# Kernel tuning notes

Measured on AMD Instinct MI355X. Metric: run time of the kernel, lower is better.

Reference implementation:

```python
import jax, jax.numpy as jnp
import numpy as np

IN_CH, OUT_CH = 32, 32
MODES1, MODES2 = 16, 16
B, H, W = 16, 256, 256


def setup_inputs() -> dict:
    key = jax.random.key(0)
    k1, k2, k3 = jax.random.split(key, 3)
    scale = 1.0 / (IN_CH * OUT_CH)
    x = jax.random.normal(k1, (B, IN_CH, H, W), dtype=jnp.float32)
    # weights stored as real view of complex: [..., 2] = (real, imag)
    w1 = scale * jax.random.uniform(k2, (IN_CH, OUT_CH, MODES1, MODES2, 2), dtype=jnp.float32)
    w2 = scale * jax.random.uniform(k3, (IN_CH, OUT_CH, MODES1, MODES2, 2), dtype=jnp.float32)
    return {"x": x, "w1": w1, "w2": w2}


def reference(x, w1, w2):
    m1, m2 = MODES1, MODES2
    b, _, h, w = x.shape
    x_ft = jnp.fft.rfft2(x, axes=(-2, -1))  # [B, in_ch, H, W//2+1] complex
    c1 = w1[..., 0] + 1j * w1[..., 1]       # [in_ch, out_ch, m1, m2]
    c2 = w2[..., 0] + 1j * w2[..., 1]
    o1 = jnp.einsum('bixy,ioxy->boxy', x_ft[:, :, :m1, :m2], c1)
    o2 = jnp.einsum('bixy,ioxy->boxy', x_ft[:, :, -m1:, :m2], c2)
    out_ft = jnp.zeros((b, c1.shape[1], h, w // 2 + 1), dtype=x_ft.dtype)
    out_ft = out_ft.at[:, :, :m1, :m2].set(o1)
    out_ft = out_ft.at[:, :, -m1:, :m2].set(o2)
    return jnp.fft.irfft2(out_ft, s=(h, w), axes=(-2, -1))
```

## Files before the change

kernel.cpp:

```cpp
#include <hip/hip_runtime.h>
#include <math.h>

#define BB 16
#define CC 32
#define HH 256
#define WW 256
#define NIMG (BB * CC)

typedef _Float16 f16;
typedef __attribute__((ext_vector_type(8))) _Float16 f16x8;
typedef __attribute__((ext_vector_type(4))) float f32x4;

constexpr float TWO_PI_OVER_256 = 6.28318530717958647692f / 256.0f;

#define N_TWF 8192
#define N_ACOL 32768
#define N_AINV 16384
#define N_BINV 8192

static __device__ __forceinline__ f32x4 mfma3(f16x8 ah, f16x8 al, f16x8 bh,
                                              f16x8 bl, f32x4 c) {
  c = __builtin_amdgcn_mfma_f32_16x16x32_f16(ah, bh, c, 0, 0, 0);
  c = __builtin_amdgcn_mfma_f32_16x16x32_f16(ah, bl, c, 0, 0, 0);
  c = __builtin_amdgcn_mfma_f32_16x16x32_f16(al, bh, c, 0, 0, 0);
  return c;
}

static __device__ __forceinline__ void split16(float v, f16* hi, f16* lo) {
  f16 h_ = (f16)v;
  *hi = h_;
  *lo = (f16)(v - (float)h_);
}

__global__ __launch_bounds__(256) void k_tw(f16* __restrict__ fb) {
  const int id = blockIdx.x * 256 + threadIdx.x;
  f16* twf_hi = fb;
  f16* twf_lo = twf_hi + N_TWF;
  f16* acol_hi = twf_lo + N_TWF;
  f16* acol_lo = acol_hi + N_ACOL;
  f16* ainv_hi = acol_lo + N_ACOL;
  f16* ainv_lo = ainv_hi + N_AINV;
  f16* binv_hi = ainv_lo + N_AINV;
  f16* binv_lo = binv_hi + N_BINV;

  float v;
  f16 *dh, *dl;
  if (id < N_TWF) {
    int idx = id;
    int j = idx & 7, lane = (idx >> 3) & 63, ks = (idx >> 9) & 7,
        nt = (idx >> 12) & 1;
    int col = nt * 16 + (lane & 15);
    int w = ks * 32 + ((lane >> 4) << 3) + j;
    int kx = col >> 1, ri = col & 1;
    int ph = (kx * w) & 255;
    float s, c;
    sincosf(TWO_PI_OVER_256 * (float)ph, &s, &c);
    v = ri ? -s : c;
    dh = twf_hi + idx;
    dl = twf_lo + idx;
  } else if (id < N_TWF + N_ACOL) {
    int idx = id - N_TWF;
    int j = idx & 7, lane = (idx >> 3) & 63, ks = (idx >> 9) & 7,
        mt = (idx >> 12) & 3, half = (idx >> 14) & 1;
    int row = mt * 16 + (lane & 15);
    int k = ks * 32 + ((lane >> 4) << 3) + j;
    int h = half * 128 + (k >> 1);
    int rj = k & 1;
    int zr = (row < 32) ? row : row - 32;
    int ky = (zr < 16) ? zr : 224 + zr;
    int ph = (ky * h) & 255;
    float s, c;
    sincosf(TWO_PI_OVER_256 * (float)ph, &s, &c);
    if (row < 32)
      v = rj ? s : c;
    else
      v = rj ? c : -s;
    dh = acol_hi + idx;
    dl = acol_lo + idx;
  } else if (id < N_TWF + N_ACOL + N_AINV) {
    int idx = id - N_TWF - N_ACOL;
    int j = idx & 7, lane = (idx >> 3) & 63, ks = (idx >> 9) & 1,
        mt = (idx >> 10) & 15;
    int h = mt * 16 + (lane & 15);
    int k = ks * 32 + ((lane >> 4) << 3) + j;
    int zr = k >> 1, rj = k & 1;
    int ky = (zr < 16) ? zr : 224 + zr;
    int ph = (ky * h) & 255;
    float s, c;
    sincosf(TWO_PI_OVER_256 * (float)ph, &s, &c);
    v = rj ? s : c;
    dh = ainv_hi + idx;
    dl = ainv_lo + idx;
  } else {
    int idx = id - N_TWF - N_ACOL - N_AINV;
    int j = idx & 7, lane = (idx >> 3) & 63, nt = (idx >> 9) & 15;
    int w = nt * 16 + (lane & 15);
    int k = ((lane >> 4) << 3) + j;
    int kx = k >> 1, ri = k & 1;
    int ph = (kx * w) & 255;
    float s, c;
    sincosf(TWO_PI_OVER_256 * (float)ph, &s, &c);
    float scale = ((kx == 0) ? 1.0f : 2.0f) / 65536.0f;
    v = ri ? -scale * s : scale * c;
    dh = binv_hi + idx;
    dl = binv_lo + idx;
  }
  f16 hi, lo;
  split16(v, &hi, &lo);
  *dh = hi;
  *dl = lo;
}

__global__ __launch_bounds__(256) void k_fwd(const float* __restrict__ x,
                                             const f16* __restrict__ twf_hi,
                                             const f16* __restrict__ twf_lo,
                                             const f16* __restrict__ acol_hi,
                                             const f16* __restrict__ acol_lo,
                                             float* __restrict__ Zp) {
  __shared__ __align__(16) f16 Yc_hi[16 * 260];
  __shared__ __align__(16) f16 Yc_lo[16 * 260];
  const int t = threadIdx.x, lane = t & 63, wid = t >> 6;
  const int l15 = lane & 15, kgrp = lane >> 4;
  const int img = blockIdx.x >> 1;
  const int half = blockIdx.x & 1;
  const float* xim = x + (size_t)img * (HH * WW) + half * 128 * WW;

  for (int r = 0; r < 2; ++r) {
    const int mt = r * 4 + wid;
    f32x4 acc0 = {0.f, 0.f, 0.f, 0.f}, acc1 = {0.f, 0.f, 0.f, 0.f};
    const float* ap = xim + (mt * 16 + l15) * WW + kgrp * 8;
    float4 st[16];
#pragma unroll
    for (int ks = 0; ks < 8; ++ks) {
      st[2 * ks] = *(const float4*)(ap + ks * 32);
      st[2 * ks + 1] = *(const float4*)(ap + ks * 32 + 4);
    }
#pragma unroll
    for (int ks = 0; ks < 8; ++ks) {
      float vv[8] = {st[2 * ks].x,     st[2 * ks].y,     st[2 * ks].z,
                     st[2 * ks].w,     st[2 * ks + 1].x, st[2 * ks + 1].y,
                     st[2 * ks + 1].z, st[2 * ks + 1].w};
      f16x8 ah, al;
#pragma unroll
      for (int e = 0; e < 8; ++e) {
        f16 h_ = (f16)vv[e];
        ah[e] = h_;
        al[e] = (f16)(vv[e] - (float)h_);
      }
      const int b0 = ((0 * 8 + ks) * 64 + lane) * 8;
      const int b1 = ((1 * 8 + ks) * 64 + lane) * 8;
      f16x8 b0h = *(const f16x8*)(twf_hi + b0);
      f16x8 b0l = *(const f16x8*)(twf_lo + b0);
      f16x8 b1h = *(const f16x8*)(twf_hi + b1);
      f16x8 b1l = *(const f16x8*)(twf_lo + b1);
      acc0 = mfma3(ah, al, b0h, b0l, acc0);
      acc1 = mfma3(ah, al, b1h, b1l, acc1);
    }
#pragma unroll
    for (int nt = 0; nt < 2; ++nt) {
#pragma unroll
      for (int jj = 0; jj < 4; ++jj) {
        const int hl = mt * 16 + kgrp * 4 + jj;
        const int n = nt * 16 + l15;
        const int kx = n >> 1, ri = n & 1;
        float v = (nt == 0) ? acc0[jj] : acc1[jj];
        f16 hv = (f16)v;
        Yc_hi[kx * 260 + 2 * hl + ri] = hv;
        Yc_lo[kx * 260 + 2 * hl + ri] = (f16)(v - (float)hv);
      }
    }
  }
  __syncthreads();
  f32x4 zacc = {0.f, 0.f, 0.f, 0.f};
#pragma unroll
  for (int ks = 0; ks < 8; ++ks) {
    const int ao = ((((half * 4 + wid) * 8) + ks) * 64 + lane) * 8;
    f16x8 a_h = *(const f16x8*)(acol_hi + ao);
    f16x8 a_l = *(const f16x8*)(acol_lo + ao);
    const int bo = l15 * 260 + ks * 32 + kgrp * 8;
    f16x8 b_h = *(const f16x8*)(Yc_hi + bo);
    f16x8 b_l = *(const f16x8*)(Yc_lo + bo);
    zacc = mfma3(a_h, a_l, b_h, b_l, zacc);
  }
  float* zp = Zp + ((size_t)img * 2 + half) * 1024;
#pragma unroll
  for (int jj = 0; jj < 4; ++jj) {
    const int row = wid * 16 + kgrp * 4 + jj;
    zp[row * 16 + l15] = zacc[jj];
  }
}

__global__ __launch_bounds__(256) void k_mix(const float* __restrict__ Zp,
                                             const float* __restrict__ w1,
                                             const float* __restrict__ w2,
                                             float* __restrict__ O) {
  __shared__ float zsr[CC][16];
  __shared__ float zsi[CC][16];
  const int t = threadIdx.x;
  const int b = blockIdx.x >> 5;
  const int zr = blockIdx.x & 31;
  const int kyi = zr & 15;
  const float* wsrc = (zr < 16) ? w1 : w2;
  {
    const int i = t >> 3, reim = (t >> 2) & 1, f4 = t & 3;
    const float* base = Zp + ((size_t)(b * CC + i) * 2) * 1024 + reim * 512 +
                        zr * 16 + f4 * 4;
    float4 a = *(const float4*)(base);
    float4 c = *(const float4*)(base + 1024);
    float4 s =
        make_float4(a.x + c.x, a.y + c.y, a.z + c.z, a.w + c.w);
    if (reim == 0)
      *(float4*)&zsr[i][f4 * 4] = s;
    else
      *(float4*)&zsi[i][f4 * 4] = s;
  }
  __syncthreads();
  const int kx = t & 15;
  const int oc0 = t >> 4;
  const float2* cp = (const float2*)wsrc;
#pragma unroll
  for (int pass = 0; pass < 2; ++pass) {
    const int oc = oc0 + pass * 16;
    float acc_r = 0.f, acc_i = 0.f;
#pragma unroll 4
    for (int i = 0; i < CC; ++i) {
      float zre = zsr[i][kx];
      float zim = zsi[i][kx];
      float2 cv = cp[(size_t)(i * CC + oc) * 256 + kyi * 16 + kx];
      acc_r += zre * cv.x - zim * cv.y;
      acc_i += zre * cv.y + zim * cv.x;
    }
    float2* dst = (float2*)O + (size_t)(b * CC + oc) * 512 + zr * 16 + kx;
    *dst = make_float2(acc_r, acc_i);
  }
}

__global__ __launch_bounds__(256) void k_inv(const float* __restrict__ O,
                                             const f16* __restrict__ ainv_hi,
                                             const f16* __restrict__ ainv_lo,
                                             const f16* __restrict__ binv_hi,
                                             const f16* __restrict__ binv_lo,
                                             float* __restrict__ out) {
  __shared__ float Olds[1024];
  __shared__ __align__(16) f16 Bf_hi[2048], Bf_lo[2048];
  __shared__ __align__(16) f16 T_hi[128 * 40], T_lo[128 * 40];
  const int t = threadIdx.x, lane = t & 63, wid = t >> 6;
  const int l15 = lane & 15, kgrp = lane >> 4;
  const int img = blockIdx.x >> 1;
  const int half = blockIdx.x & 1;
  {
    float4 v = ((const float4*)(O + (size_t)img * 1024))[t];
    *(float4*)&Olds[t * 4] = v;
  }
  __syncthreads();
#pragma unroll
  for (int e = 0; e < 8; ++e) {
    const int idx = e * 256 + t;
    const int nt = idx >> 10, ks = (idx >> 9) & 1, ln = (idx >> 3) & 63,
              j = idx & 7;
    const int k = ks * 32 + ((ln >> 4) << 3) + j;
    const int n = nt * 16 + (ln & 15);
    const int zr = k >> 1, rj = k & 1, kx = n >> 1, ri = n & 1;
    const float Or = Olds[(zr * 16 + kx) * 2];
    const float Oi = Olds[(zr * 16 + kx) * 2 + 1];
    const float v = (rj == 0) ? (ri == 0 ? Or : Oi) : (ri == 0 ? -Oi : Or);
    f16 hv = (f16)v;
    Bf_hi[idx] = hv;
    Bf_lo[idx] = (f16)(v - (float)hv);
  }
  __syncthreads();
#pragma unroll
  for (int mm = 0; mm < 2; ++mm) {
    const int mtl = wid * 2 + mm;
    const int mt = half * 8 + mtl;
    f32x4 acc0 = {0.f, 0.f, 0.f, 0.f}, acc1 = {0.f, 0.f, 0.f, 0.f};
#pragma unroll
    for (int ks = 0; ks < 2; ++ks) {
      const int ao = ((mt * 2 + ks) * 64 + lane) * 8;
      f16x8 a_h = *(const f16x8*)(ainv_hi + ao);
      f16x8 a_l = *(const f16x8*)(ainv_lo + ao);
      const int bo0 = ((0 * 2 + ks) * 64 + lane) * 8;
      const int bo1 = ((1 * 2 + ks) * 64 + lane) * 8;
      f16x8 b0h = *(const f16x8*)(Bf_hi + bo0);
      f16x8 b0l = *(const f16x8*)(Bf_lo + bo0);
      f16x8 b1h = *(const f16x8*)(Bf_hi + bo1);
      f16x8 b1l = *(const f16x8*)(Bf_lo + bo1);
      acc0 = mfma3(a_h, a_l, b0h, b0l, acc0);
      acc1 = mfma3(a_h, a_l, b1h, b1l, acc1);
    }
#pragma unroll
    for (int nt = 0; nt < 2; ++nt) {
#pragma unroll
      for (int jj = 0; jj < 4; ++jj) {
        const int hl = mtl * 16 + kgrp * 4 + jj;
        const int n = nt * 16 + l15;
        float v = (nt == 0) ? acc0[jj] : acc1[jj];
        f16 hv = (f16)v;
        T_hi[hl * 40 + n] = hv;
        T_lo[hl * 40 + n] = (f16)(v - (float)hv);
      }
    }
  }
  __syncthreads();
  float* op = out + (size_t)img * (HH * WW) + (size_t)half * 128 * WW;
#pragma unroll
  for (int mm = 0; mm < 2; ++mm) {
    const int mtl = wid * 2 + mm;
    const int ao = (mtl * 16 + l15) * 40 + kgrp * 8;
    f16x8 a_h = *(const f16x8*)(T_hi + ao);
    f16x8 a_l = *(const f16x8*)(T_lo + ao);
#pragma unroll 4
    for (int nt = 0; nt < 16; ++nt) {
      const int bo = (nt * 64 + lane) * 8;
      f16x8 b_h = *(const f16x8*)(binv_hi + bo);
      f16x8 b_l = *(const f16x8*)(binv_lo + bo);
      f32x4 acc = {0.f, 0.f, 0.f, 0.f};
      acc = mfma3(a_h, a_l, b_h, b_l, acc);
#pragma unroll
      for (int jj = 0; jj < 4; ++jj) {
        const int hl = mtl * 16 + kgrp * 4 + jj;
        op[(size_t)hl * WW + nt * 16 + l15] = acc[jj];
      }
    }
  }
}

extern "C" void kernel_launch(void* const* d_in, const int* in_sizes, int n_in,
                              void* d_out, int out_size, void* d_ws,
                              size_t ws_size, hipStream_t stream) {
  const float* x = (const float*)d_in[0];
  const float* w1 = (const float*)d_in[1];
  const float* w2 = (const float*)d_in[2];
  float* out = (float*)d_out;

  f16* fb = (f16*)d_ws;
  f16* twf_hi = fb;
  f16* twf_lo = twf_hi + N_TWF;
  f16* acol_hi = twf_lo + N_TWF;
  f16* acol_lo = acol_hi + N_ACOL;
  f16* ainv_hi = acol_lo + N_ACOL;
  f16* ainv_lo = ainv_hi + N_AINV;
  f16* binv_hi = ainv_lo + N_AINV;
  f16* binv_lo = binv_hi + N_BINV;
  float* Zp = (float*)(binv_lo + N_BINV);
  float* O = Zp + (size_t)NIMG * 2048;

  k_tw<<<dim3(256), dim3(256), 0, stream>>>(fb);
  k_fwd<<<dim3(NIMG * 2), dim3(256), 0, stream>>>(x, twf_hi, twf_lo, acol_hi,
                                                  acol_lo, Zp);
  k_mix<<<dim3(BB * 32), dim3(256), 0, stream>>>(Zp, w1, w2, O);
  k_inv<<<dim3(NIMG * 2), dim3(256), 0, stream>>>(O, ainv_hi, ainv_lo, binv_hi,
                                                  binv_lo, out);
}
```

Measured before the change: 78.66 us.

## Double-buffer input rows into LDS with async loads and swizzled layout

The forward kernel now streams the input half-image into LDS in 32-row chunks using global_load_lds, double-buffered so later chunks load while earlier ones are run through MFMA. Work is redistributed so each wave owns one of two twiddle column tiles, kept in registers for the whole kernel instead of reloaded per step. LDS layouts for both the staged input and the intermediate Yc buffer use XOR swizzles in place of padding to avoid bank conflicts. The cost is 64KB of extra LDS per block, which may lower occupancy, plus manual waitcnt and barrier synchronisation.

```diff
diff --git a/kernel.cpp b/kernel.cpp
--- a/kernel.cpp
+++ b/kernel.cpp
@@ -117,69 +117,101 @@
                                              const f16* __restrict__ acol_hi,
                                              const f16* __restrict__ acol_lo,
                                              float* __restrict__ Zp) {
-  __shared__ __align__(16) f16 Yc_hi[16 * 260];
-  __shared__ __align__(16) f16 Yc_lo[16 * 260];
+  __shared__ __align__(16) float xs[2][32][256];
+  __shared__ __align__(16) f16 Yc_hi[16 * 256];
+  __shared__ __align__(16) f16 Yc_lo[16 * 256];
   const int t = threadIdx.x, lane = t & 63, wid = t >> 6;
   const int l15 = lane & 15, kgrp = lane >> 4;
   const int img = blockIdx.x >> 1;
   const int half = blockIdx.x & 1;
   const float* xim = x + (size_t)img * (HH * WW) + half * 128 * WW;
-
-  for (int r = 0; r < 2; ++r) {
-    const int mt = r * 4 + wid;
-    f32x4 acc0 = {0.f, 0.f, 0.f, 0.f}, acc1 = {0.f, 0.f, 0.f, 0.f};
-    const float* ap = xim + (mt * 16 + l15) * WW + kgrp * 8;
-    float4 st[16];
-#pragma unroll
-    for (int ks = 0; ks < 8; ++ks) {
-      st[2 * ks] = *(const float4*)(ap + ks * 32);
-      st[2 * ks + 1] = *(const float4*)(ap + ks * 32 + 4);
-    }
-#pragma unroll
-    for (int ks = 0; ks < 8; ++ks) {
-      float vv[8] = {st[2 * ks].x,     st[2 * ks].y,     st[2 * ks].z,
-                     st[2 * ks].w,     st[2 * ks + 1].x, st[2 * ks + 1].y,
-                     st[2 * ks + 1].z, st[2 * ks + 1].w};
-      f16x8 ah, al;
-#pragma unroll
-      for (int e = 0; e < 8; ++e) {
-        f16 h_ = (f16)vv[e];
-        ah[e] = h_;
-        al[e] = (f16)(vv[e] - (float)h_);
+  const int mt = wid >> 1;
+  const int nt = wid & 1;
+
+  f16x8 tbh[8], tbl[8];
+#pragma unroll
+  for (int ks = 0; ks < 8; ++ks) {
+    const int bo = ((nt * 8 + ks) * 64 + lane) * 8;
+    tbh[ks] = *(const f16x8*)(twf_hi + bo);
+    tbl[ks] = *(const f16x8*)(twf_lo + bo);
+  }
+  asm volatile("" ::: "memory");
+
+  auto STAGE = [&](int c, int b) {
+#pragma unroll
+    for (int i = 0; i < 8; ++i) {
+      const int row = wid * 8 + i;
+      const int go = (lane * 16) ^ ((row & 7) << 4);
+      __builtin_amdgcn_global_load_lds(
+          (const __attribute__((address_space(1))) void*)(xim +
+                                                          (c * 32 + row) * WW +
+                                                          (go >> 2)),
+          (__attribute__((address_space(3))) void*)&xs[b][row][0], 16, 0, 0);
+    }
+  };
+
+  STAGE(0, 0);
+  STAGE(1, 1);
+
+#pragma unroll
+  for (int c = 0; c < 4; ++c) {
+    if (c == 3)
+      asm volatile("s_waitcnt vmcnt(0)" ::: "memory");
+    else
+      asm volatile("s_waitcnt vmcnt(8)" ::: "memory");
+    __builtin_amdgcn_s_barrier();
+    {
+      const int row = mt * 16 + l15;
+      const char* rb = (const char*)&xs[c & 1][row][0];
+      const int swz = (row & 7) << 4;
+      f32x4 acc = {0.f, 0.f, 0.f, 0.f};
+#pragma unroll
+      for (int ks = 0; ks < 8; ++ks) {
+        const int off = 128 * ks + 32 * kgrp;
+        float4 a0 = *(const float4*)(rb + (off ^ swz));
+        float4 a1 = *(const float4*)(rb + ((off + 16) ^ swz));
+        float vv[8] = {a0.x, a0.y, a0.z, a0.w, a1.x, a1.y, a1.z, a1.w};
+        f16x8 ah, al;
+#pragma unroll
+        for (int e = 0; e < 8; ++e) {
+          f16 h_ = (f16)vv[e];
+          ah[e] = h_;
+          al[e] = (f16)(vv[e] - (float)h_);
+        }
+        acc = mfma3(ah, al, tbh[ks], tbl[ks], acc);
       }
-      const int b0 = ((0 * 8 + ks) * 64 + lane) * 8;
-      const int b1 = ((1 * 8 + ks) * 64 + lane) * 8;
-      f16x8 b0h = *(const f16x8*)(twf_hi + b0);
-      f16x8 b0l = *(const f16x8*)(twf_lo + b0);
-      f16x8 b1h = *(const f16x8*)(twf_hi + b1);
-      f16x8 b1l = *(const f16x8*)(twf_lo + b1);
-      acc0 = mfma3(ah, al, b0h, b0l, acc0);
-      acc1 = mfma3(ah, al, b1h, b1l, acc1);
-    }
-#pragma unroll
-    for (int nt = 0; nt < 2; ++nt) {
+      const int n = nt * 16 + l15;
+      const int kx = n >> 1, ri = n & 1;
+      char* yh = (char*)Yc_hi + kx * 512;
+      char* yl = (char*)Yc_lo + kx * 512;
+      const int kswz = (kx & 7) << 4;
 #pragma unroll
       for (int jj = 0; jj < 4; ++jj) {
-        const int hl = mt * 16 + kgrp * 4 + jj;
-        const int n = nt * 16 + l15;
-        const int kx = n >> 1, ri = n & 1;
-        float v = (nt == 0) ? acc0[jj] : acc1[jj];
+        const int hl = c * 32 + mt * 16 + kgrp * 4 + jj;
+        const int boff = (4 * hl + 2 * ri) ^ kswz;
+        float v = acc[jj];
         f16 hv = (f16)v;
-        Yc_hi[kx * 260 + 2 * hl + ri] = hv;
-        Yc_lo[kx * 260 + 2 * hl + ri] = (f16)(v - (float)hv);
+        *(f16*)(yh + boff) = hv;
+        *(f16*)(yl + boff) = (f16)(v - (float)hv);
       }
     }
-  }
-  __syncthreads();
+    asm volatile("s_waitcnt lgkmcnt(0)" ::: "memory");
+    __builtin_amdgcn_s_barrier();
+    if (c < 2) STAGE(c + 2, c & 1);
+  }
+
   f32x4 zacc = {0.f, 0.f, 0.f, 0.f};
+  const int kswz2 = (l15 & 7) << 4;
+  const char* ybh = (const char*)Yc_hi + l15 * 512;
+  const char* ybl = (const char*)Yc_lo + l15 * 512;
 #pragma unroll
   for (int ks = 0; ks < 8; ++ks) {
     const int ao = ((((half * 4 + wid) * 8) + ks) * 64 + lane) * 8;
     f16x8 a_h = *(const f16x8*)(acol_hi + ao);
     f16x8 a_l = *(const f16x8*)(acol_lo + ao);
-    const int bo = l15 * 260 + ks * 32 + kgrp * 8;
-    f16x8 b_h = *(const f16x8*)(Yc_hi + bo);
-    f16x8 b_l = *(const f16x8*)(Yc_lo + bo);
+    const int boff = (64 * ks + 16 * kgrp) ^ kswz2;
+    f16x8 b_h = *(const f16x8*)(ybh + boff);
+    f16x8 b_l = *(const f16x8*)(ybl + boff);
     zacc = mfma3(a_h, a_l, b_h, b_l, zacc);
   }
   float* zp = Zp + ((size_t)img * 2 + half) * 1024;
@@ -207,8 +239,7 @@
                         zr * 16 + f4 * 4;
     float4 a = *(const float4*)(base);
     float4 c = *(const float4*)(base + 1024);
-    float4 s =
-        make_float4(a.x + c.x, a.y + c.y, a.z + c.z, a.w + c.w);
+    float4 s = make_float4(a.x + c.x, a.y + c.y, a.z + c.z, a.w + c.w);
     if (reim == 0)
       *(float4*)&zsr[i][f4 * 4] = s;
     else
```

Result: no change. 77.34 us (-1.7%).
